# Kernel optimization log

Measured on AMD Instinct MI355X. Metric: run time of the kernel, lower is better.

The kernel has to match this reference:

```python
import jax, jax.numpy as jnp
import numpy as np

B, C_IN, C_BOT, H = 256, 48, 8, 4096
SCALE = 1.0 / np.sqrt(8.0).astype(np.float32)


def setup_inputs() -> dict:
    key = jax.random.key(0)
    k1, k2, k3 = jax.random.split(key, 3)
    x = jax.random.normal(k1, (B, C_IN, H, 1), dtype=jnp.float32)
    # 1x1 conv weights, stored as [out_channels, in_channels]
    w_down = jax.random.normal(k2, (C_BOT, C_IN), dtype=jnp.float32) * (1.0 / np.sqrt(C_IN))
    w_up = jax.random.normal(k3, (C_IN, C_BOT), dtype=jnp.float32) * (1.0 / np.sqrt(C_BOT))
    return {"x": x, "w_down": w_down, "w_up": w_up}


def reference(x, w_down, w_up):
    # x: [B, 48, H, 1] -> [B, 48, H]
    xs = jnp.squeeze(x, axis=3)
    # fc_down applied (identically) for k, q, v: same weights, same input
    kqv = jnp.einsum('oc,bch->boh', w_down, xs)  # [B, 8, H]
    # attention matrix over channel dim: [B, 8, 8]
    am = jax.nn.softmax(jnp.einsum('bih,bjh->bij', kqv, kqv) * SCALE, axis=-1)
    z = jnp.einsum('bij,bjh->bih', am, kqv)       # [B, 8, H]
    out = jnp.einsum('co,boh->bch', w_up, z)      # [B, 48, H]
    return out[..., None]                          # [B, 48, H, 1]
```

## Files before the change

kernel.cpp:

```cpp
#include <hip/hip_runtime.h>

#define B_    256
#define CIN   48
#define CBOT  8
#define H_    4096
#define SCALE_ 0.35355339059327373f

__global__ __launch_bounds__(1024) void ultimus_kernel(
    const float* __restrict__ x,
    const float* __restrict__ w_down,
    const float* __restrict__ w_up,
    float* __restrict__ out)
{
    const int b = blockIdx.x;
    const int t = threadIdx.x;

    __shared__ float s_wdT[CIN * CBOT];
    __shared__ float s_wu [CIN * CBOT];
    __shared__ float s_red[16 * 36];
    __shared__ float s_am [CBOT * CBOT];

    if (t < CIN * CBOT) {
        const int c = t >> 3, o = t & 7;
        s_wdT[t] = w_down[o * CIN + c];
        s_wu[t]  = w_up[t];
    }
    __syncthreads();

    const float* xb = x + (size_t)b * (CIN * H_);
    const int h0 = t << 2;

    float kqv[CBOT][4];
    #pragma unroll
    for (int o = 0; o < CBOT; ++o)
        kqv[o][0] = kqv[o][1] = kqv[o][2] = kqv[o][3] = 0.0f;

    #pragma unroll 8
    for (int c = 0; c < CIN; ++c) {
        const float4 xv = *reinterpret_cast<const float4*>(xb + c * H_ + h0);
        #pragma unroll
        for (int o = 0; o < CBOT; ++o) {
            const float w = s_wdT[c * CBOT + o];
            kqv[o][0] += w * xv.x;
            kqv[o][1] += w * xv.y;
            kqv[o][2] += w * xv.z;
            kqv[o][3] += w * xv.w;
        }
    }

    float g[36];
    {
        int idx = 0;
        #pragma unroll
        for (int i = 0; i < CBOT; ++i) {
            #pragma unroll
            for (int j = i; j < CBOT; ++j, ++idx) {
                g[idx] = kqv[i][0] * kqv[j][0] + kqv[i][1] * kqv[j][1]
                       + kqv[i][2] * kqv[j][2] + kqv[i][3] * kqv[j][3];
            }
        }
    }
    #pragma unroll
    for (int k = 0; k < 36; ++k) {
        float v = g[k];
        v += __shfl_down(v, 32, 64);
        v += __shfl_down(v, 16, 64);
        v += __shfl_down(v,  8, 64);
        v += __shfl_down(v,  4, 64);
        v += __shfl_down(v,  2, 64);
        v += __shfl_down(v,  1, 64);
        g[k] = v;
    }
    const int wave = t >> 6;
    const int lane = t & 63;
    if (lane == 0) {
        #pragma unroll
        for (int k = 0; k < 36; ++k) s_red[wave * 36 + k] = g[k];
    }
    __syncthreads();

    if (t < 36) {
        float v = 0.0f;
        #pragma unroll
        for (int w = 0; w < 16; ++w) v += s_red[w * 36 + t];
        s_red[t] = v;
    }
    __syncthreads();

    if (t < 8) {
        float row[8];
        #pragma unroll
        for (int j = 0; j < 8; ++j) {
            const int i2 = t < j ? t : j;
            const int j2 = t < j ? j : t;
            const int tri = i2 * 8 - (i2 * (i2 - 1)) / 2 + (j2 - i2);
            row[j] = s_red[tri] * SCALE_;
        }
        float m = row[0];
        #pragma unroll
        for (int j = 1; j < 8; ++j) m = fmaxf(m, row[j]);
        float s = 0.0f;
        #pragma unroll
        for (int j = 0; j < 8; ++j) { row[j] = __expf(row[j] - m); s += row[j]; }
        const float inv = 1.0f / s;
        #pragma unroll
        for (int j = 0; j < 8; ++j) s_am[t * 8 + j] = row[j] * inv;
    }
    __syncthreads();

    float z[CBOT][4];
    #pragma unroll
    for (int o = 0; o < CBOT; ++o) {
        float a0 = 0.f, a1 = 0.f, a2 = 0.f, a3 = 0.f;
        #pragma unroll
        for (int j = 0; j < CBOT; ++j) {
            const float a = s_am[o * 8 + j];
            a0 += a * kqv[j][0];
            a1 += a * kqv[j][1];
            a2 += a * kqv[j][2];
            a3 += a * kqv[j][3];
        }
        z[o][0] = a0; z[o][1] = a1; z[o][2] = a2; z[o][3] = a3;
    }

    float* ob = out + (size_t)b * (CIN * H_);
    #pragma unroll 8
    for (int c = 0; c < CIN; ++c) {
        float4 r;
        r.x = r.y = r.z = r.w = 0.0f;
        #pragma unroll
        for (int o = 0; o < CBOT; ++o) {
            const float w = s_wu[c * CBOT + o];
            r.x += w * z[o][0];
            r.y += w * z[o][1];
            r.z += w * z[o][2];
            r.w += w * z[o][3];
        }
        *reinterpret_cast<float4*>(ob + c * H_ + h0) = r;
    }
}

extern "C" void kernel_launch(void* const* d_in, const int* in_sizes, int n_in,
                              void* d_out, int out_size, void* d_ws, size_t ws_size,
                              hipStream_t stream) {
    const float* x      = (const float*)d_in[0];
    const float* w_down = (const float*)d_in[1];
    const float* w_up   = (const float*)d_in[2];
    float* out          = (float*)d_out;

    hipLaunchKernelGGL(ultimus_kernel, dim3(B_), dim3(1024), 0, stream,
                       x, w_down, w_up, out);
}
```

Baseline: 379.5 us.

## Split fused kernel into down/gram and up passes across H chunks

```diff
diff --git a/kernel.cpp b/kernel.cpp
--- a/kernel.cpp
+++ b/kernel.cpp
@@ -6,29 +6,33 @@
 #define H_    4096
 #define SCALE_ 0.35355339059327373f
 
-__global__ __launch_bounds__(1024) void ultimus_kernel(
+#define SPLIT    8
+#define CHUNK    (H_ / SPLIT)
+#define THREADS  128
+
+template <bool STORE_KQV>
+__global__ __launch_bounds__(THREADS) void k_down(
     const float* __restrict__ x,
     const float* __restrict__ w_down,
-    const float* __restrict__ w_up,
-    float* __restrict__ out)
+    float* __restrict__ ws_kqv,
+    float* __restrict__ ws_gram)
 {
-    const int b = blockIdx.x;
+    const int blk = blockIdx.x;
+    const int b = blk / SPLIT;
+    const int s = blk % SPLIT;
     const int t = threadIdx.x;
 
     __shared__ float s_wdT[CIN * CBOT];
-    __shared__ float s_wu [CIN * CBOT];
-    __shared__ float s_red[16 * 36];
-    __shared__ float s_am [CBOT * CBOT];
-
-    if (t < CIN * CBOT) {
-        const int c = t >> 3, o = t & 7;
-        s_wdT[t] = w_down[o * CIN + c];
-        s_wu[t]  = w_up[t];
-    }
-    __syncthreads();
-
+    __shared__ float s_red[2 * 36];
+
+    for (int i = t; i < CIN * CBOT; i += THREADS) {
+        const int c = i >> 3, o = i & 7;
+        s_wdT[i] = w_down[o * CIN + c];
+    }
+    __syncthreads();
+
+    const int h0 = s * CHUNK + (t << 2);
     const float* xb = x + (size_t)b * (CIN * H_);
-    const int h0 = t << 2;
 
     float kqv[CBOT][4];
     #pragma unroll
@@ -48,17 +52,24 @@
         }
     }
 
+    if (STORE_KQV) {
+        float* kb = ws_kqv + (size_t)b * (CBOT * H_);
+        #pragma unroll
+        for (int o = 0; o < CBOT; ++o) {
+            float4 v = make_float4(kqv[o][0], kqv[o][1], kqv[o][2], kqv[o][3]);
+            *reinterpret_cast<float4*>(kb + o * H_ + h0) = v;
+        }
+    }
+
     float g[36];
     {
         int idx = 0;
         #pragma unroll
-        for (int i = 0; i < CBOT; ++i) {
+        for (int i = 0; i < CBOT; ++i)
             #pragma unroll
-            for (int j = i; j < CBOT; ++j, ++idx) {
+            for (int j = i; j < CBOT; ++j, ++idx)
                 g[idx] = kqv[i][0] * kqv[j][0] + kqv[i][1] * kqv[j][1]
                        + kqv[i][2] * kqv[j][2] + kqv[i][3] * kqv[j][3];
-            }
-        }
     }
     #pragma unroll
     for (int k = 0; k < 36; ++k) {
@@ -71,19 +82,47 @@
         v += __shfl_down(v,  1, 64);
         g[k] = v;
     }
-    const int wave = t >> 6;
-    const int lane = t & 63;
+    const int wave = t >> 6, lane = t & 63;
     if (lane == 0) {
         #pragma unroll
         for (int k = 0; k < 36; ++k) s_red[wave * 36 + k] = g[k];
     }
     __syncthreads();
-
+    if (t < 36) ws_gram[(size_t)blk * 36 + t] = s_red[t] + s_red[36 + t];
+}
+
+template <bool LOAD_KQV>
+__global__ __launch_bounds__(THREADS) void k_up(
+    const float* __restrict__ x,
+    const float* __restrict__ w_down,
+    const float* __restrict__ ws_kqv,
+    const float* __restrict__ ws_gram,
+    const float* __restrict__ w_up,
+    float* __restrict__ out)
+{
+    const int blk = blockIdx.x;
+    const int b = blk / SPLIT;
+    const int s = blk % SPLIT;
+    const int t = threadIdx.x;
+
+    __shared__ float s_wu[CIN * CBOT];
+    __shared__ float s_wdT[CIN * CBOT];
+    __shared__ float s_g[36];
+    __shared__ float s_am[CBOT * CBOT];
+
+    for (int i = t; i < CIN * CBOT; i += THREADS) {
+        s_wu[i] = w_up[i];
+        if (!LOAD_KQV) {
+            const int c = i >> 3, o = i & 7;
+            s_wdT[i] = w_down[o * CIN + c];
+        }
+    }
     if (t < 36) {
         float v = 0.0f;
         #pragma unroll
-        for (int w = 0; w < 16; ++w) v += s_red[w * 36 + t];
-        s_red[t] = v;
+        for (int ss = 0; ss < SPLIT; ++ss)
+            v += ws_gram[(size_t)(b * SPLIT + ss) * 36 + t];
+        s_g[t] = v;
     }
     __syncthreads();
 
@@ -94,19 +133,48 @@
             const int i2 = t < j ? t : j;
             const int j2 = t < j ? j : t;
             const int tri = i2 * 8 - (i2 * (i2 - 1)) / 2 + (j2 - i2);
-            row[j] = s_red[tri] * SCALE_;
+            row[j] = s_g[tri] * SCALE_;
         }
         float m = row[0];
         #pragma unroll
         for (int j = 1; j < 8; ++j) m = fmaxf(m, row[j]);
-        float s = 0.0f;
-        #pragma unroll
-        for (int j = 0; j < 8; ++j) { row[j] = __expf(row[j] - m); s += row[j]; }
-        const float inv = 1.0f / s;
+        float sum = 0.0f;
+        #pragma unroll
+        for (int j = 0; j < 8; ++j) { row[j] = __expf(row[j] - m); sum += row[j]; }
+        const float inv = 1.0f / sum;
         #pragma unroll
         for (int j = 0; j < 8; ++j) s_am[t * 8 + j] = row[j] * inv;
     }
     __syncthreads();
+
+    const int h0 = s * CHUNK + (t << 2);
+
+    float kqv[CBOT][4];
+    if (LOAD_KQV) {
+        const float* kb = ws_kqv + (size_t)b * (CBOT * H_);
+        #pragma unroll
+        for (int o = 0; o < CBOT; ++o) {
+            const float4 v = *reinterpret_cast<const float4*>(kb + o * H_ + h0);
+            kqv[o][0] = v.x; kqv[o][1] = v.y; kqv[o][2] = v.z; kqv[o][3] = v.w;
+        }
+    } else {
+        const float* xb = x + (size_t)b * (CIN * H_);
+        #pragma unroll
+        for (int o = 0; o < CBOT; ++o)
+            kqv[o][0] = kqv[o][1] = kqv[o][2] = kqv[o][3] = 0.0f;
+        #pragma unroll 8
+        for (int c = 0; c < CIN; ++c) {
+            const float4 xv = *reinterpret_cast<const float4*>(xb + c * H_ + h0);
+            #pragma unroll
+            for (int o = 0; o < CBOT; ++o) {
+                const float w = s_wdT[c * CBOT + o];
+                kqv[o][0] += w * xv.x;
+                kqv[o][1] += w * xv.y;
+                kqv[o][2] += w * xv.z;
+                kqv[o][3] += w * xv.w;
+            }
+        }
+    }
 
     float z[CBOT][4];
     #pragma unroll
@@ -148,6 +216,25 @@
     const float* w_up   = (const float*)d_in[2];
     float* out          = (float*)d_out;
 
-    hipLaunchKernelGGL(ultimus_kernel, dim3(B_), dim3(1024), 0, stream,
-                       x, w_down, w_up, out);
+    const size_t kqv_elems  = (size_t)B_ * CBOT * H_;
+    const size_t gram_elems = (size_t)B_ * SPLIT * 36;
+    const size_t need_bytes = (kqv_elems + gram_elems) * sizeof(float);
+
+    const dim3 grid(B_ * SPLIT);
+    const dim3 block(THREADS);
+
+    if (ws_size >= need_bytes) {
+        float* ws_kqv  = (float*)d_ws;
+        float* ws_gram = ws_kqv + kqv_elems;
+        hipLaunchKernelGGL((k_down<true>),  grid, block, 0, stream,
+                           x, w_down, ws_kqv, ws_gram);
+        hipLaunchKernelGGL((k_up<true>),    grid, block, 0, stream,
+                           x, w_down, ws_kqv, ws_gram, w_up, out);
+    } else {
+        float* ws_gram = (float*)d_ws;
+        hipLaunchKernelGGL((k_down<false>), grid, block, 0, stream,
+                           x, w_down, nullptr, ws_gram);
+        hipLaunchKernelGGL((k_up<false>),   grid, block, 0, stream,
+                           x, w_down, nullptr, ws_gram, w_up, out);
+    }
 }
```

After: 390.3 us. 2.8% more time.
